# Performance work log

Hardware: AMD Instinct MI355X
Metric: run time of the kernel (lower is better)

## Reference

```python
import jax, jax.numpy as jnp
import numpy as np

N_NODES = 50000
N_EDGES = 800000
D = 256


def _mean_aggregate(x, src, tgt, num_nodes):
    # scatter-mean of source features onto target nodes: [N, D]
    summed = jax.ops.segment_sum(x[src], tgt, num_segments=num_nodes)
    count = jax.ops.segment_sum(jnp.ones((src.shape[0],), x.dtype), tgt,
                                num_segments=num_nodes)
    return summed / jnp.maximum(count, 1.0)[:, None]


def _sage_conv(x, src, tgt, W_l, b, W_r):
    # PyG SAGEConv (aggr='mean'): lin_l(mean_j x_j) + lin_r(x_i)
    agg = _mean_aggregate(x, src, tgt, x.shape[0])
    return agg @ W_l + b + x @ W_r


def setup_inputs() -> dict:
    key = jax.random.key(0)
    ks = jax.random.split(key, 8)
    s = 1.0 / np.sqrt(D)
    x = jax.random.normal(ks[0], (N_NODES, D), dtype=jnp.float32)
    edge_index = jax.random.randint(ks[1], (2, N_EDGES), 0, N_NODES, dtype=jnp.int64)
    return {
        "x": x,
        "edge_index": edge_index,
        "W1_l": jax.random.normal(ks[2], (D, D), dtype=jnp.float32) * s,
        "b1": jnp.zeros((D,), dtype=jnp.float32),
        "W1_r": jax.random.normal(ks[3], (D, D), dtype=jnp.float32) * s,
        "W2_l": jax.random.normal(ks[4], (D, D), dtype=jnp.float32) * s,
        "b2": jnp.zeros((D,), dtype=jnp.float32),
        "W2_r": jax.random.normal(ks[5], (D, D), dtype=jnp.float32) * s,
    }


def reference(x, edge_index, W1_l, b1, W1_r, W2_l, b2, W2_r):
    src, tgt = edge_index[0], edge_index[1]
    h = jax.nn.relu(_sage_conv(x, src, tgt, W1_l, b1, W1_r))
    return _sage_conv(h, src, tgt, W2_l, b2, W2_r)
```

## Files before the change

### kernel.cpp

```cpp
#include <hip/hip_runtime.h>
#include <hip/hip_bf16.h>

#define NN 50000
#define NE 800000
#define DD 256
#define KK 512
#define PAD 64
#define CSTR 16

#define FB 3125
#define CB 12500
#define WB 1024
#define PREP_GRID (2 * FB + (CB - FB) + WB)

typedef unsigned short u16;
typedef unsigned int   u32;
typedef unsigned char  u8;
typedef __attribute__((ext_vector_type(8))) __bf16 bf16x8;
typedef __attribute__((ext_vector_type(4))) float  f32x4;
typedef __attribute__((ext_vector_type(2))) float  f32x2;
typedef __attribute__((ext_vector_type(8))) u16    u16x8;
typedef __attribute__((ext_vector_type(4))) u16    u16x4;

#define GLOAD_LDS16(g, l) \
  __builtin_amdgcn_global_load_lds((const __attribute__((address_space(1))) void*)(g), \
                                   (__attribute__((address_space(3))) void*)(l), 16, 0, 0)

static __device__ __forceinline__ u16 f2bf(float f) {
  u32 u = __float_as_uint(f);
  u32 r = (u + 0x7FFFu + ((u >> 16) & 1u)) >> 16;
  return (u16)r;
}

__global__ void k_prep(const int* __restrict__ src, const int* __restrict__ tgt,
                       int* __restrict__ cnt, int* __restrict__ col,
                       const float* __restrict__ x, u16* __restrict__ x_bf,
                       u32* __restrict__ x_f8,
                       const float* __restrict__ W1l, const float* __restrict__ W1r,
                       const float* __restrict__ W2l, const float* __restrict__ W2r,
                       u16* __restrict__ Wc1T, u16* __restrict__ Wc2T) {
  const int b = blockIdx.x;
  int role, idx;
  if (b < 2 * FB) {
    role = b & 1;
    idx = b >> 1;
  } else if (b < 2 * FB + (CB - FB)) {
    role = 1;
    idx = FB + (b - 2 * FB);
  } else {
    role = 2;
    idx = b - (2 * FB + (CB - FB));
  }

  if (role == 0) {
    int i = idx * 256 + threadIdx.x;
    int t = tgt[i];
    int p = atomicAdd(&cnt[t * CSTR], 1);
    if (p < PAD) col[t * PAD + p] = src[i];
  } else if (role == 1) {
    int i = idx * 256 + threadIdx.x;
    const float4 v = *reinterpret_cast<const float4*>(x + i * 4);
    u16x4 o; o.x = f2bf(v.x); o.y = f2bf(v.y); o.z = f2bf(v.z); o.w = f2bf(v.w);
    *reinterpret_cast<u16x4*>(x_bf + i * 4) = o;
    int pk = __builtin_amdgcn_cvt_pk_fp8_f32(v.x, v.y, 0, false);
    pk = __builtin_amdgcn_cvt_pk_fp8_f32(v.z, v.w, pk, true);
    x_f8[i] = (u32)pk;
  } else {
    int gid = idx * 256 + threadIdx.x;
    int layer = gid >> 17;
    int idx2 = gid & 131071;
    int n = idx2 >> 9, k = idx2 & 511;
    const float* Wl = layer ? W2l : W1l;
    const float* Wr = layer ? W2r : W1r;
    u16* WcT = layer ? Wc2T : Wc1T;
    float v = (k < DD) ? Wl[k * DD + n] : Wr[(k - DD) * DD + n];
    int reg = k >> 6, ko = k & 63;
    int k2 = (reg << 6) + ((((ko >> 3) ^ (n & 7)) << 3)) + (ko & 7);
    WcT[n * KK + k2] = f2bf(v);
  }
}

__global__ void k_aggregate(const u8* __restrict__ feat8, const int* __restrict__ cnt,
                            const int* __restrict__ col, u16* __restrict__ out) {
  const int wave = threadIdx.x >> 6;
  const int lane = threadIdx.x & 63;
  const int half = lane >> 5;
  const int l32 = lane & 31;
  const int node = blockIdx.x * 4 + wave;
  int deg = cnt[node * CSTR];
  if (deg > PAD) deg = PAD;
  const int s = node * PAD, e = s + deg;
  const int fo = l32 * 8;
  float a[8] = {0.f, 0.f, 0.f, 0.f, 0.f, 0.f, 0.f, 0.f};

#define ACC8(vv)                                                       \
  {                                                                    \
    f32x2 p0 = __builtin_amdgcn_cvt_pk_f32_fp8((int)(vv).x, false);    \
    f32x2 p1 = __builtin_amdgcn_cvt_pk_f32_fp8((int)(vv).x, true);     \
    f32x2 p2 = __builtin_amdgcn_cvt_pk_f32_fp8((int)(vv).y, false);    \
    f32x2 p3 = __builtin_amdgcn_cvt_pk_f32_fp8((int)(vv).y, true);     \
    a[0] += p0.x; a[1] += p0.y; a[2] += p1.x; a[3] += p1.y;            \
    a[4] += p2.x; a[5] += p2.y; a[6] += p3.x; a[7] += p3.y;            \
  }

  int i = s + half;
  for (; i + 6 < e; i += 8) {
    int c0 = col[i], c1 = col[i + 2], c2 = col[i + 4], c3 = col[i + 6];
    uint2 v0 = *reinterpret_cast<const uint2*>(feat8 + c0 * DD + fo);
    uint2 v1 = *reinterpret_cast<const uint2*>(feat8 + c1 * DD + fo);
    uint2 v2 = *reinterpret_cast<const uint2*>(feat8 + c2 * DD + fo);
    uint2 v3 = *reinterpret_cast<const uint2*>(feat8 + c3 * DD + fo);
    ACC8(v0) ACC8(v1) ACC8(v2) ACC8(v3)
  }
  for (; i < e; i += 2) {
    uint2 v = *reinterpret_cast<const uint2*>(feat8 + col[i] * DD + fo);
    ACC8(v)
  }
#undef ACC8
#pragma unroll
  for (int j = 0; j < 8; ++j) a[j] += __shfl_xor(a[j], 32, 64);

  if (half == 0) {
    const float scale = (deg > 0) ? 1.0f / (float)deg : 0.0f;
    u16x8 o;
#pragma unroll
    for (int j = 0; j < 8; ++j) o[j] = f2bf(a[j] * scale);
    *reinterpret_cast<u16x8*>(out + node * DD + fo) = o;
  }
}

#define BM 64
#define BN 256
#define BK 64

template <int LAYER>
__global__ void k_gemm_fused(const u16* __restrict__ A0, const u16* __restrict__ A1,
                             const u16* __restrict__ WcT, const float* __restrict__ bias,
                             u16* __restrict__ outb, u8* __restrict__ outf8,
                             float* __restrict__ outf, int M) {
  __shared__ alignas(16) u16 lA[BM * BK];
  __shared__ alignas(16) u16 lB[BN * BK];
  const int tid = threadIdx.x;
  const int rowBase = blockIdx.x * BM;
  const int wave = tid >> 6, lane = tid & 63;
  const int wc = wave;
  const int l8 = lane >> 3;
  const int ch = lane & 7;

  f32x4 acc[4][4] = {};

  for (int k0 = 0; k0 < KK; k0 += BK) {
    if (k0) __syncthreads();
    const u16* Asrc = (k0 < DD) ? A0 : A1;
    const int kk = k0 & (DD - 1);
#pragma unroll
    for (int j = 0; j < 2; ++j) {
      int row = wave * 16 + j * 8 + l8;
      const u16* g = Asrc + (size_t)(rowBase + row) * DD + kk + ((ch ^ (row & 7)) << 3);
      GLOAD_LDS16(g, &lA[(wave * 16 + j * 8) * BK]);
    }
#pragma unroll
    for (int j = 0; j < 8; ++j) {
      int row = wave * 64 + j * 8 + l8;
      const u16* g = WcT + (size_t)row * KK + k0 + (ch << 3);
      GLOAD_LDS16(g, &lB[(wave * 64 + j * 8) * BK]);
    }
    __syncthreads();

#pragma unroll
    for (int ks = 0; ks < 2; ++ks) {
      const int kbyte = ks * 64 + (lane >> 4) * 16;
      bf16x8 af[4], bfg[4];
#pragma unroll
      for (int m = 0; m < 4; ++m) {
        int row = m * 16 + (lane & 15);
        af[m] = *reinterpret_cast<const bf16x8*>((const char*)lA + row * 128 + (kbyte ^ ((row & 7) << 4)));
      }
#pragma unroll
      for (int n = 0; n < 4; ++n) {
        int row = wc * 64 + n * 16 + (lane & 15);
        bfg[n] = *reinterpret_cast<const bf16x8*>((const char*)lB + row * 128 + (kbyte ^ ((row & 7) << 4)));
      }
#pragma unroll
      for (int m = 0; m < 4; ++m)
#pragma unroll
        for (int n = 0; n < 4; ++n)
          acc[m][n] = __builtin_amdgcn_mfma_f32_16x16x32_bf16(af[m], bfg[n], acc[m][n], 0, 0, 0);
    }
  }

  const int lrow = (lane >> 4) * 4;
  const int lcol = lane & 15;
#pragma unroll
  for (int n = 0; n < 4; ++n) {
    const int gcol = wc * 64 + n * 16 + lcol;
    const float bv = bias[gcol];
#pragma unroll
    for (int m = 0; m < 4; ++m) {
#pragma unroll
      for (int r = 0; r < 4; ++r) {
        const int grow = rowBase + m * 16 + lrow + r;
        if (grow < M) {
          float v = acc[m][n][r] + bv;
          if (LAYER == 1) {
            v = fmaxf(v, 0.0f);
            outb[grow * DD + gcol] = f2bf(v);
            int pk = __builtin_amdgcn_cvt_pk_fp8_f32(v, 0.0f, 0, false);
            outf8[grow * DD + gcol] = (u8)(pk & 0xff);
          } else {
            outf[grow * DD + gcol] = v;
          }
        }
      }
    }
  }
}

extern "C" void kernel_launch(void* const* d_in, const int* in_sizes, int n_in,
                              void* d_out, int out_size, void* d_ws, size_t ws_size,
                              hipStream_t stream) {
  const float* x    = (const float*)d_in[0];
  const int*   ei   = (const int*)d_in[1];
  const float* W1l  = (const float*)d_in[2];
  const float* b1   = (const float*)d_in[3];
  const float* W1r  = (const float*)d_in[4];
  const float* W2l  = (const float*)d_in[5];
  const float* b2   = (const float*)d_in[6];
  const float* W2r  = (const float*)d_in[7];
  float* out = (float*)d_out;

  const int* srcIdx = ei;
  const int* tgtIdx = ei + NE;

  char* ws = (char*)d_ws;
  int* cnt    = (int*)(ws + 0);
  int* col    = (int*)(ws + 3200000);
  u16* x_bf   = (u16*)(ws + 16000000);
  u16* h_bf   = (u16*)(ws + 41600000);
  u16* agg_bf = (u16*)(ws + 67200000);
  u8*  x_f8   = (u8*) (ws + 92800000);
  u8*  h_f8   = (u8*) (ws + 105600000);
  u16* Wc1T   = (u16*)(ws + 118400000);
  u16* Wc2T   = (u16*)(ws + 118662144);

  hipMemsetAsync(cnt, 0, NN * CSTR * sizeof(int), stream);
  k_prep<<<PREP_GRID, 256, 0, stream>>>(srcIdx, tgtIdx, cnt, col, x, x_bf,
                                        (u32*)x_f8,
                                        W1l, W1r, W2l, W2r, Wc1T, Wc2T);

  const int ggrid = (NN + BM - 1) / BM;

  k_aggregate<<<NN / 4, 256, 0, stream>>>(x_f8, cnt, col, agg_bf);
  k_gemm_fused<1><<<ggrid, 256, 0, stream>>>(agg_bf, x_bf, Wc1T, b1, h_bf, h_f8, nullptr, NN);
  k_aggregate<<<NN / 4, 256, 0, stream>>>(h_f8, cnt, col, agg_bf);
  k_gemm_fused<2><<<ggrid, 256, 0, stream>>>(agg_bf, h_bf, Wc2T, b2, nullptr, nullptr, out, NN);
}
```

Measured before the change: 190.0 us.

## Fuse neighbor mean-aggregation into the GEMM kernel via LDS-resident aggregate tile

Removes the separate aggregation kernels and computes each block's 64-row aggregated feature tile directly into shared memory, where the GEMM then reads it for the first half of K. This avoids writing and re-reading the bf16 aggregate buffer through global memory and saves two kernel launches. The trade-off is that each wave gathers 16 nodes serially with one lane per 4 features, which gives less memory-level parallelism than the old dedicated kernel. LDS use also rises to about 72KB per block, limiting occupancy, and the gather cannot overlap with the MFMA phase inside a block.

```diff
diff --git a/kernel.cpp b/kernel.cpp
--- a/kernel.cpp
+++ b/kernel.cpp
@@ -42,14 +42,11 @@
   const int b = blockIdx.x;
   int role, idx;
   if (b < 2 * FB) {
-    role = b & 1;
-    idx = b >> 1;
+    role = b & 1;  idx = b >> 1;
   } else if (b < 2 * FB + (CB - FB)) {
-    role = 1;
-    idx = FB + (b - 2 * FB);
+    role = 1;      idx = FB + (b - 2 * FB);
   } else {
-    role = 2;
-    idx = b - (2 * FB + (CB - FB));
+    role = 2;      idx = b - (2 * FB + (CB - FB));
   }
 
   if (role == 0) {
@@ -80,66 +77,20 @@
   }
 }
 
-__global__ void k_aggregate(const u8* __restrict__ feat8, const int* __restrict__ cnt,
-                            const int* __restrict__ col, u16* __restrict__ out) {
-  const int wave = threadIdx.x >> 6;
-  const int lane = threadIdx.x & 63;
-  const int half = lane >> 5;
-  const int l32 = lane & 31;
-  const int node = blockIdx.x * 4 + wave;
-  int deg = cnt[node * CSTR];
-  if (deg > PAD) deg = PAD;
-  const int s = node * PAD, e = s + deg;
-  const int fo = l32 * 8;
-  float a[8] = {0.f, 0.f, 0.f, 0.f, 0.f, 0.f, 0.f, 0.f};
-
-#define ACC8(vv)                                                       \
-  {                                                                    \
-    f32x2 p0 = __builtin_amdgcn_cvt_pk_f32_fp8((int)(vv).x, false);    \
-    f32x2 p1 = __builtin_amdgcn_cvt_pk_f32_fp8((int)(vv).x, true);     \
-    f32x2 p2 = __builtin_amdgcn_cvt_pk_f32_fp8((int)(vv).y, false);    \
-    f32x2 p3 = __builtin_amdgcn_cvt_pk_f32_fp8((int)(vv).y, true);     \
-    a[0] += p0.x; a[1] += p0.y; a[2] += p1.x; a[3] += p1.y;            \
-    a[4] += p2.x; a[5] += p2.y; a[6] += p3.x; a[7] += p3.y;            \
-  }
-
-  int i = s + half;
-  for (; i + 6 < e; i += 8) {
-    int c0 = col[i], c1 = col[i + 2], c2 = col[i + 4], c3 = col[i + 6];
-    uint2 v0 = *reinterpret_cast<const uint2*>(feat8 + c0 * DD + fo);
-    uint2 v1 = *reinterpret_cast<const uint2*>(feat8 + c1 * DD + fo);
-    uint2 v2 = *reinterpret_cast<const uint2*>(feat8 + c2 * DD + fo);
-    uint2 v3 = *reinterpret_cast<const uint2*>(feat8 + c3 * DD + fo);
-    ACC8(v0) ACC8(v1) ACC8(v2) ACC8(v3)
-  }
-  for (; i < e; i += 2) {
-    uint2 v = *reinterpret_cast<const uint2*>(feat8 + col[i] * DD + fo);
-    ACC8(v)
-  }
-#undef ACC8
-#pragma unroll
-  for (int j = 0; j < 8; ++j) a[j] += __shfl_xor(a[j], 32, 64);
-
-  if (half == 0) {
-    const float scale = (deg > 0) ? 1.0f / (float)deg : 0.0f;
-    u16x8 o;
-#pragma unroll
-    for (int j = 0; j < 8; ++j) o[j] = f2bf(a[j] * scale);
-    *reinterpret_cast<u16x8*>(out + node * DD + fo) = o;
-  }
-}
-
 #define BM 64
 #define BN 256
 #define BK 64
 
 template <int LAYER>
-__global__ void k_gemm_fused(const u16* __restrict__ A0, const u16* __restrict__ A1,
-                             const u16* __restrict__ WcT, const float* __restrict__ bias,
-                             u16* __restrict__ outb, u8* __restrict__ outf8,
-                             float* __restrict__ outf, int M) {
-  __shared__ alignas(16) u16 lA[BM * BK];
-  __shared__ alignas(16) u16 lB[BN * BK];
+__launch_bounds__(256, 2)
+__global__ void k_layer(const u8* __restrict__ feat8, const int* __restrict__ cnt,
+                        const int* __restrict__ col, const u16* __restrict__ A1,
+                        const u16* __restrict__ WcT, const float* __restrict__ bias,
+                        u16* __restrict__ outb, u8* __restrict__ outf8,
+                        float* __restrict__ outf, int M) {
+  __shared__ alignas(16) u16 lAg[64 * 256];
+  __shared__ alignas(16) u16 lAx[64 * 64];
+  __shared__ alignas(16) u16 lB[256 * 64];
   const int tid = threadIdx.x;
   const int rowBase = blockIdx.x * BM;
   const int wave = tid >> 6, lane = tid & 63;
@@ -147,17 +98,64 @@
   const int l8 = lane >> 3;
   const int ch = lane & 7;
 
+  const int fo = lane * 4;
+  const int wbyte = (lane >> 4) * 128 +
+                    (((((lane & 15) >> 1) ^ 0) << 4) | ((lane & 1) << 3));
+#pragma unroll 1
+  for (int n = 0; n < 16; ++n) {
+    const int row = wave * 16 + n;
+    const int node = rowBase + row;
+    int deg = (node < M) ? cnt[node * CSTR] : 0;
+    if (deg > PAD) deg = PAD;
+    const int base = node * PAD;
+    f32x4 a = {0.f, 0.f, 0.f, 0.f};
+    int e = 0;
+    for (; e + 3 < deg; e += 4) {
+      int c0 = col[base + e],     c1 = col[base + e + 1];
+      int c2 = col[base + e + 2], c3 = col[base + e + 3];
+      u32 v0 = *reinterpret_cast<const u32*>(feat8 + (size_t)c0 * DD + fo);
+      u32 v1 = *reinterpret_cast<const u32*>(feat8 + (size_t)c1 * DD + fo);
+      u32 v2 = *reinterpret_cast<const u32*>(feat8 + (size_t)c2 * DD + fo);
+      u32 v3 = *reinterpret_cast<const u32*>(feat8 + (size_t)c3 * DD + fo);
+      f32x2 p;
+      p = __builtin_amdgcn_cvt_pk_f32_fp8((int)v0, false); a.x += p.x; a.y += p.y;
+      p = __builtin_amdgcn_cvt_pk_f32_fp8((int)v0, true);  a.z += p.x; a.w += p.y;
+      p = __builtin_amdgcn_cvt_pk_f32_fp8((int)v1, false); a.x += p.x; a.y += p.y;
+      p = __builtin_amdgcn_cvt_pk_f32_fp8((int)v1, true);  a.z += p.x; a.w += p.y;
+      p = __builtin_amdgcn_cvt_pk_f32_fp8((int)v2, false); a.x += p.x; a.y += p.y;
+      p = __builtin_amdgcn_cvt_pk_f32_fp8((int)v2, true);  a.z += p.x; a.w += p.y;
+      p = __builtin_amdgcn_cvt_pk_f32_fp8((int)v3, false); a.x += p.x; a.y += p.y;
+      p = __builtin_amdgcn_cvt_pk_f32_fp8((int)v3, true);  a.z += p.x; a.w += p.y;
+    }
+    for (; e < deg; ++e) {
+      u32 v = *reinterpret_cast<const u32*>(feat8 + (size_t)col[base + e] * DD + fo);
+      f32x2 p;
+      p = __builtin_amdgcn_cvt_pk_f32_fp8((int)v, false); a.x += p.x; a.y += p.y;
+      p = __builtin_amdgcn_cvt_pk_f32_fp8((int)v, true);  a.z += p.x; a.w += p.y;
+    }
+    const float scale = (deg > 0) ? 1.0f / (float)deg : 0.0f;
+    u16x4 o;
+    o.x = f2bf(a.x * scale); o.y = f2bf(a.y * scale);
+    o.z = f2bf(a.z * scale); o.w = f2bf(a.w * scale);
+    int byte = (wbyte & ~0x70) | ((wbyte & 0x70) ^ ((row & 7) << 4));
+    *reinterpret_cast<u16x4*>((char*)lAg + row * 512 + byte) = o;
+  }
+
   f32x4 acc[4][4] = {};
 
   for (int k0 = 0; k0 < KK; k0 += BK) {
+    const bool isAgg = (k0 < DD);
     if (k0) __syncthreads();
-    const u16* Asrc = (k0 < DD) ? A0 : A1;
-    const int kk = k0 & (DD - 1);
-#pragma unroll
-    for (int j = 0; j < 2; ++j) {
-      int row = wave * 16 + j * 8 + l8;
-      const u16* g = Asrc + (size_t)(rowBase + row) * DD + kk + ((ch ^ (row & 7)) << 3);
-      GLOAD_LDS16(g, &lA[(wave * 16 + j * 8) * BK]);
+    if (!isAgg) {
+      const int kk = k0 - DD;
+#pragma unroll
+      for (int j = 0; j < 2; ++j) {
+        int row = wave * 16 + j * 8 + l8;
+        int grow = rowBase + row;
+        int gr = (grow < M) ? grow : 0;
+        const u16* g = A1 + (size_t)gr * DD + kk + ((ch ^ (row & 7)) << 3);
+        GLOAD_LDS16(g, &lAx[(wave * 16 + j * 8) * BK]);
+      }
     }
 #pragma unroll
     for (int j = 0; j < 8; ++j) {
@@ -174,7 +172,10 @@
 #pragma unroll
       for (int m = 0; m < 4; ++m) {
         int row = m * 16 + (lane & 15);
-        af[m] = *reinterpret_cast<const bf16x8*>((const char*)lA + row * 128 + (kbyte ^ ((row & 7) << 4)));
+        int sw = kbyte ^ ((row & 7) << 4);
+        af[m] = isAgg
+          ? *reinterpret_cast<const bf16x8*>((const char*)lAg + row * 512 + (k0 << 1) + sw)
+          : *reinterpret_cast<const bf16x8*>((const char*)lAx + row * 128 + sw);
       }
 #pragma unroll
       for (int n = 0; n < 4; ++n) {
@@ -237,11 +238,10 @@
   int* col    = (int*)(ws + 3200000);
   u16* x_bf   = (u16*)(ws + 16000000);
   u16* h_bf   = (u16*)(ws + 41600000);
-  u16* agg_bf = (u16*)(ws + 67200000);
-  u8*  x_f8   = (u8*) (ws + 92800000);
-  u8*  h_f8   = (u8*) (ws + 105600000);
-  u16* Wc1T   = (u16*)(ws + 118400000);
-  u16* Wc2T   = (u16*)(ws + 118662144);
+  u8*  x_f8   = (u8*) (ws + 67200000);
+  u8*  h_f8   = (u8*) (ws + 80000000);
+  u16* Wc1T   = (u16*)(ws + 92800000);
+  u16* Wc2T   = (u16*)(ws + 93062144);
 
   hipMemsetAsync(cnt, 0, NN * CSTR * sizeof(int), stream);
   k_prep<<<PREP_GRID, 256, 0, stream>>>(srcIdx, tgtIdx, cnt, col, x, x_bf,
@@ -250,8 +250,8 @@
 
   const int ggrid = (NN + BM - 1) / BM;
 
-  k_aggregate<<<NN / 4, 256, 0, stream>>>(x_f8, cnt, col, agg_bf);
-  k_gemm_fused<1><<<ggrid, 256, 0, stream>>>(agg_bf, x_bf, Wc1T, b1, h_bf, h_f8, nullptr, NN);
-  k_aggregate<<<NN / 4, 256, 0, stream>>>(h_f8, cnt, col, agg_bf);
-  k_gemm_fused<2><<<ggrid, 256, 0, stream>>>(agg_bf, h_bf, Wc2T, b2, nullptr, nullptr, out, NN);
-}
+  k_layer<1><<<ggrid, 256, 0, stream>>>(x_f8, cnt, col, x_bf, Wc1T, b1,
+                                        h_bf, h_f8, nullptr, NN);
+  k_layer<2><<<ggrid, 256, 0, stream>>>(h_f8, cnt, col, h_bf, Wc2T, b2,
+                                        nullptr, nullptr, out, NN);
+}
```

New measurement: 359.2 us. 1.89x slower.
